# Kernel tuning notes

Measured on AMD Instinct MI355X. Metric: run time of the kernel, lower is better.

Reference implementation:

```python
import jax, jax.numpy as jnp
import numpy as np

MAXDIS = 1e-3   # squared-distance threshold for edge acceptance
COUNT = 5       # interpolation points per segment
EPS_ABS = 1e-5  # added per-coordinate before sqrt in vector norm


def setup_inputs() -> dict:
    key = jax.random.key(0)
    k1, k2 = jax.random.split(key)
    recon_points = jax.random.uniform(k1, (16, 17, 2), dtype=jnp.float32)
    gt_points = jax.random.uniform(k2, (16, 4096, 2), dtype=jnp.float32)
    return {"recon_points": recon_points, "gt_points": gt_points}


def _edge_mask(p1, p2):
    # For every keypoint pair (i, j), sample COUNT points on the segment
    # start=p1[:,i], end=p1[:,j]:  K = start*t + end*(1-t), t in linspace(0,1,COUNT).
    B, N, D = p1.shape
    t = jnp.linspace(0.0, 1.0, COUNT).astype(p1.dtype)          # [C]
    K = (p1[:, :, None, None, :] * t[None, None, None, :, None]
         + p1[:, None, :, None, :] * (1.0 - t)[None, None, None, :, None])  # [B,N,N,C,D]
    # Squared distances to gt points via ||K||^2 + ||p2||^2 - 2 K.p2^T (avoids [.,.,M,D] blowup)
    k2 = jnp.sum(K * K, axis=-1)                                  # [B,N,N,C]
    g2 = jnp.sum(p2 * p2, axis=-1)                                # [B,M]
    cross = jnp.einsum('bijcd,bmd->bijcm', K, p2)                 # [B,N,N,C,M]
    d2 = k2[..., None] + g2[:, None, None, None, :] - 2.0 * cross
    cdis = jnp.mean(jnp.min(d2, axis=-1), axis=-1)                # [B,N,N]: mean over C of min over M
    # Edges only for i > j (original loops j in range(i)); squared-dist threshold.
    tril = jnp.tril(jnp.ones((N, N), dtype=bool), k=-1)
    return (cdis < MAXDIS) & tril[None, :, :]                     # [B,N,N]


def reference(recon_points, gt_points):
    p1, p2 = recon_points, gt_points
    B, N, D = p1.shape
    mask = _edge_mask(p1, p2).astype(p1.dtype)                    # [B,N,N]
    # Flattened vector index k<N corresponds to pair (0, k): u_k = p1[:,0] - p1[:,k].
    u = p1[:, :1, :] - p1                                         # [B,N,D]
    dot = jnp.abs(jnp.einsum('bid,bjd->bij', u, u))               # [B,N,N]
    absu = jnp.sqrt(jnp.sum(u * u + EPS_ABS, axis=-1))            # [B,N]  (= sqrt(||u||^2 + D*eps))
    abs_dot = absu[:, :, None] * absu[:, None, :]                 # [B,N,N]
    abs_dot = jnp.where(abs_dot == 0, jnp.ones_like(abs_dot), abs_dot)
    cos = dot * mask / abs_dot
    idx_num = 1.0 + jnp.sum(mask)                                 # 1 + total edge count
    return jnp.sum(cos) / idx_num
```

## Files before the change

kernel.cpp:

```cpp
#include <hip/hip_runtime.h>
#include <math.h>

#define BATCH 16
#define NPTS 17
#define MPTS 4096
#define NPAIR 136
#define NPAIRS_TOTAL (BATCH * NPAIR)
#define CNT 5
#define MAXDIS 1e-3f
#define EPS_ABS 1e-5f

__global__ __launch_bounds__(256) void pair_kernel(const float* __restrict__ recon,
                                                   const float* __restrict__ gt,
                                                   float2* __restrict__ slots) {
    const int blk = blockIdx.x;
    const int wave = threadIdx.x >> 6;
    const int lane = threadIdx.x & 63;
    const int b = blk / NPAIR;
    const int p = blk - b * NPAIR;
    int i = 1;
    while ((i * (i + 1)) / 2 <= p) ++i;
    const int j = p - (i * (i - 1)) / 2;

    const float* rp = recon + b * NPTS * 2;
    const float pix = rp[2 * i], piy = rp[2 * i + 1];
    const float pjx = rp[2 * j], pjy = rp[2 * j + 1];

    const float ex = pix - pjx, ey = piy - pjy;
    const float e2x = 2.0f * ex, e2y = 2.0f * ey;
    const float E = ex * ex + ey * ey;

    float ms0 = 1e30f, ms1 = 1e30f, ms2 = 1e30f, ms3 = 1e30f, ms4 = 1e30f;

    const float4* g4 = (const float4*)(gt + (size_t)b * MPTS * 2);
    #pragma unroll
    for (int it = 0; it < 8; ++it) {
        const float4 g = g4[threadIdx.x + (it << 8)];
        const float dxa = pjx - g.x, dya = pjy - g.y;
        const float Aa = fmaf(dxa, dxa, dya * dya);
        const float Ba = fmaf(e2x, dxa, e2y * dya);
        const float dxb = pjx - g.z, dyb = pjy - g.w;
        const float Ab = fmaf(dxb, dxb, dyb * dyb);
        const float Bb = fmaf(e2x, dxb, e2y * dyb);

        ms0 = fminf(ms0, fminf(Aa, Ab));
        ms1 = fminf(ms1, fminf(fmaf(0.25f, Ba, Aa), fmaf(0.25f, Bb, Ab)));
        ms2 = fminf(ms2, fminf(fmaf(0.50f, Ba, Aa), fmaf(0.50f, Bb, Ab)));
        ms3 = fminf(ms3, fminf(fmaf(0.75f, Ba, Aa), fmaf(0.75f, Bb, Ab)));
        ms4 = fminf(ms4, fminf(Aa + Ba, Ab + Bb));
    }

    #pragma unroll
    for (int off = 32; off > 0; off >>= 1) {
        ms0 = fminf(ms0, __shfl_xor(ms0, off, 64));
        ms1 = fminf(ms1, __shfl_xor(ms1, off, 64));
        ms2 = fminf(ms2, __shfl_xor(ms2, off, 64));
        ms3 = fminf(ms3, __shfl_xor(ms3, off, 64));
        ms4 = fminf(ms4, __shfl_xor(ms4, off, 64));
    }

    __shared__ float part[4][CNT];
    if (lane == 0) {
        part[wave][0] = ms0;
        part[wave][1] = ms1;
        part[wave][2] = ms2;
        part[wave][3] = ms3;
        part[wave][4] = ms4;
    }
    __syncthreads();

    if (threadIdx.x == 0) {
        float m[CNT];
        #pragma unroll
        for (int c = 0; c < CNT; ++c)
            m[c] = fminf(fminf(part[0][c], part[1][c]),
                         fminf(part[2][c], part[3][c]));
        const float m0 = m[0];
        const float m1 = fmaf(0.0625f, E, m[1]);
        const float m2 = fmaf(0.25f, E, m[2]);
        const float m3 = fmaf(0.5625f, E, m[3]);
        const float m4 = m[4] + E;
        const float cdis = ((((m0 + m1) + m2) + m3) + m4) / 5.0f;

        float cosv = 0.0f, cntv = 0.0f;
        if (cdis < MAXDIS) {
            const float u0x = rp[0], u0y = rp[1];
            const float uix = u0x - pix, uiy = u0y - piy;
            const float ujx = u0x - pjx, ujy = u0y - pjy;
            const float dot = fabsf(uix * ujx + uiy * ujy);
            const float ai = sqrtf((uix * uix + EPS_ABS) + (uiy * uiy + EPS_ABS));
            const float aj = sqrtf((ujx * ujx + EPS_ABS) + (ujy * ujy + EPS_ABS));
            cosv = dot / (ai * aj);
            cntv = 1.0f;
        }
        slots[blk] = make_float2(cosv, cntv);
    }
}

__global__ __launch_bounds__(64) void reduce_kernel(const float2* __restrict__ slots,
                                                    float* __restrict__ out) {
    const int lane = threadIdx.x;
    float c = 0.0f, n = 0.0f;
    #pragma unroll
    for (int m = 0; m < NPAIRS_TOTAL / 64; ++m) {
        const float2 w = slots[lane + 64 * m];
        c += w.x;
        n += w.y;
    }
    #pragma unroll
    for (int off = 32; off > 0; off >>= 1) {
        c += __shfl_xor(c, off, 64);
        n += __shfl_xor(n, off, 64);
    }
    if (lane == 0) out[0] = c / (1.0f + n);
}

extern "C" void kernel_launch(void* const* d_in, const int* in_sizes, int n_in,
                              void* d_out, int out_size, void* d_ws, size_t ws_size,
                              hipStream_t stream) {
    const float* recon = (const float*)d_in[0];
    const float* gt = (const float*)d_in[1];
    float* out = (float*)d_out;
    float2* slots = (float2*)d_ws;

    pair_kernel<<<NPAIRS_TOTAL, 256, 0, stream>>>(recon, gt, slots);
    reduce_kernel<<<1, 64, 0, stream>>>(slots, out);
}
```

Measured before the change: 13.23 us.

## Compute endpoint min-distances once per keypoint instead of per pair

The t=0 and t=1 sample minima depend only on a single keypoint, so they are now computed once per keypoint by extra blocks and looked up in the reduce kernel. Pair blocks now track only the three interior samples, which cuts per-element work in the hot loop. In exchange there are 272 extra blocks, larger slot records, and the threshold test plus indexed gathers move into the single-block reduce. The summation order of cdis changes slightly.

Result: slower. 14.99 us (+13.3%).

```diff
diff --git a/kernel.cpp b/kernel.cpp
--- a/kernel.cpp
+++ b/kernel.cpp
@@ -6,16 +6,49 @@
 #define MPTS 4096
 #define NPAIR 136
 #define NPAIRS_TOTAL (BATCH * NPAIR)
-#define CNT 5
+#define NKEY (BATCH * NPTS)
+#define NBLK (NPAIRS_TOTAL + NKEY)
 #define MAXDIS 1e-3f
 #define EPS_ABS 1e-5f
 
 __global__ __launch_bounds__(256) void pair_kernel(const float* __restrict__ recon,
                                                    const float* __restrict__ gt,
-                                                   float2* __restrict__ slots) {
+                                                   float4* __restrict__ slots,
+                                                   float* __restrict__ pmin) {
     const int blk = blockIdx.x;
     const int wave = threadIdx.x >> 6;
     const int lane = threadIdx.x & 63;
+
+    if (blk >= NPAIRS_TOTAL) {
+        const int k = blk - NPAIRS_TOTAL;
+        const int b = k / NPTS;
+        const int pt = k - b * NPTS;
+        const float px = recon[b * NPTS * 2 + 2 * pt];
+        const float py = recon[b * NPTS * 2 + 2 * pt + 1];
+
+        float mn = 1e30f;
+        const float4* g4 = (const float4*)(gt + (size_t)b * MPTS * 2);
+        #pragma unroll
+        for (int it = 0; it < 8; ++it) {
+            const float4 g = g4[threadIdx.x + (it << 8)];
+            const float dxa = px - g.x, dya = py - g.y;
+            const float dxb = px - g.z, dyb = py - g.w;
+            const float Aa = fmaf(dxa, dxa, dya * dya);
+            const float Ab = fmaf(dxb, dxb, dyb * dyb);
+            mn = fminf(mn, fminf(Aa, Ab));
+        }
+        #pragma unroll
+        for (int off = 32; off > 0; off >>= 1)
+            mn = fminf(mn, __shfl_xor(mn, off, 64));
+
+        __shared__ float kpart[4];
+        if (lane == 0) kpart[wave] = mn;
+        __syncthreads();
+        if (threadIdx.x == 0)
+            pmin[k] = fminf(fminf(kpart[0], kpart[1]), fminf(kpart[2], kpart[3]));
+        return;
+    }
+
     const int b = blk / NPAIR;
     const int p = blk - b * NPAIR;
     int i = 1;
@@ -30,7 +63,7 @@
     const float e2x = 2.0f * ex, e2y = 2.0f * ey;
     const float E = ex * ex + ey * ey;
 
-    float ms0 = 1e30f, ms1 = 1e30f, ms2 = 1e30f, ms3 = 1e30f, ms4 = 1e30f;
+    float ms1 = 1e30f, ms2 = 1e30f, ms3 = 1e30f;
 
     const float4* g4 = (const float4*)(gt + (size_t)b * MPTS * 2);
     #pragma unroll
@@ -43,69 +76,67 @@
         const float Ab = fmaf(dxb, dxb, dyb * dyb);
         const float Bb = fmaf(e2x, dxb, e2y * dyb);
 
-        ms0 = fminf(ms0, fminf(Aa, Ab));
         ms1 = fminf(ms1, fminf(fmaf(0.25f, Ba, Aa), fmaf(0.25f, Bb, Ab)));
         ms2 = fminf(ms2, fminf(fmaf(0.50f, Ba, Aa), fmaf(0.50f, Bb, Ab)));
         ms3 = fminf(ms3, fminf(fmaf(0.75f, Ba, Aa), fmaf(0.75f, Bb, Ab)));
-        ms4 = fminf(ms4, fminf(Aa + Ba, Ab + Bb));
     }
 
     #pragma unroll
     for (int off = 32; off > 0; off >>= 1) {
-        ms0 = fminf(ms0, __shfl_xor(ms0, off, 64));
         ms1 = fminf(ms1, __shfl_xor(ms1, off, 64));
         ms2 = fminf(ms2, __shfl_xor(ms2, off, 64));
         ms3 = fminf(ms3, __shfl_xor(ms3, off, 64));
-        ms4 = fminf(ms4, __shfl_xor(ms4, off, 64));
     }
 
-    __shared__ float part[4][CNT];
+    __shared__ float part[4][3];
     if (lane == 0) {
-        part[wave][0] = ms0;
-        part[wave][1] = ms1;
-        part[wave][2] = ms2;
-        part[wave][3] = ms3;
-        part[wave][4] = ms4;
+        part[wave][0] = ms1;
+        part[wave][1] = ms2;
+        part[wave][2] = ms3;
     }
     __syncthreads();
 
     if (threadIdx.x == 0) {
-        float m[CNT];
-        #pragma unroll
-        for (int c = 0; c < CNT; ++c)
-            m[c] = fminf(fminf(part[0][c], part[1][c]),
-                         fminf(part[2][c], part[3][c]));
-        const float m0 = m[0];
-        const float m1 = fmaf(0.0625f, E, m[1]);
-        const float m2 = fmaf(0.25f, E, m[2]);
-        const float m3 = fmaf(0.5625f, E, m[3]);
-        const float m4 = m[4] + E;
-        const float cdis = ((((m0 + m1) + m2) + m3) + m4) / 5.0f;
+        const float r1 = fminf(fminf(part[0][0], part[1][0]), fminf(part[2][0], part[3][0]));
+        const float r2 = fminf(fminf(part[0][1], part[1][1]), fminf(part[2][1], part[3][1]));
+        const float r3 = fminf(fminf(part[0][2], part[1][2]), fminf(part[2][2], part[3][2]));
+        const float m1 = fmaf(0.0625f, E, r1);
+        const float m2 = fmaf(0.25f, E, r2);
+        const float m3 = fmaf(0.5625f, E, r3);
+        const float s123 = (m1 + m2) + m3;
 
-        float cosv = 0.0f, cntv = 0.0f;
-        if (cdis < MAXDIS) {
-            const float u0x = rp[0], u0y = rp[1];
-            const float uix = u0x - pix, uiy = u0y - piy;
-            const float ujx = u0x - pjx, ujy = u0y - pjy;
-            const float dot = fabsf(uix * ujx + uiy * ujy);
-            const float ai = sqrtf((uix * uix + EPS_ABS) + (uiy * uiy + EPS_ABS));
-            const float aj = sqrtf((ujx * ujx + EPS_ABS) + (ujy * ujy + EPS_ABS));
-            cosv = dot / (ai * aj);
-            cntv = 1.0f;
-        }
-        slots[blk] = make_float2(cosv, cntv);
+        const float u0x = rp[0], u0y = rp[1];
+        const float uix = u0x - pix, uiy = u0y - piy;
+        const float ujx = u0x - pjx, ujy = u0y - pjy;
+        const float dot = fabsf(uix * ujx + uiy * ujy);
+        const float ai = sqrtf((uix * uix + EPS_ABS) + (uiy * uiy + EPS_ABS));
+        const float aj = sqrtf((ujx * ujx + EPS_ABS) + (ujy * ujy + EPS_ABS));
+        const float cosv = dot / (ai * aj);
+
+        float4 s;
+        s.x = cosv;
+        s.y = s123;
+        s.z = __int_as_float(b * NPTS + i);
+        s.w = __int_as_float(b * NPTS + j);
+        slots[blk] = s;
     }
 }
 
-__global__ __launch_bounds__(64) void reduce_kernel(const float2* __restrict__ slots,
+__global__ __launch_bounds__(64) void reduce_kernel(const float4* __restrict__ slots,
+                                                    const float* __restrict__ pmin,
                                                     float* __restrict__ out) {
     const int lane = threadIdx.x;
     float c = 0.0f, n = 0.0f;
     #pragma unroll
     for (int m = 0; m < NPAIRS_TOTAL / 64; ++m) {
-        const float2 w = slots[lane + 64 * m];
-        c += w.x;
-        n += w.y;
+        const float4 s = slots[lane + 64 * m];
+        const float pmi = pmin[__float_as_int(s.z)];
+        const float pmj = pmin[__float_as_int(s.w)];
+        const float cdis = ((pmj + s.y) + pmi) / 5.0f;
+        if (cdis < MAXDIS) {
+            c += s.x;
+            n += 1.0f;
+        }
     }
     #pragma unroll
     for (int off = 32; off > 0; off >>= 1) {
@@ -121,8 +152,9 @@
     const float* recon = (const float*)d_in[0];
     const float* gt = (const float*)d_in[1];
     float* out = (float*)d_out;
-    float2* slots = (float2*)d_ws;
+    float4* slots = (float4*)d_ws;
+    float* pmin = (float*)((char*)d_ws + (size_t)NPAIRS_TOTAL * 16);
 
-    pair_kernel<<<NPAIRS_TOTAL, 256, 0, stream>>>(recon, gt, slots);
-    reduce_kernel<<<1, 64, 0, stream>>>(slots, out);
+    pair_kernel<<<NBLK, 256, 0, stream>>>(recon, gt, slots, pmin);
+    reduce_kernel<<<1, 64, 0, stream>>>(slots, pmin, out);
 }
```
